# Kernel optimization log

Hardware: AMD Instinct MI355X
Metric: run time of the kernel (lower is better)

The kernel has to match this reference:

```python
import jax, jax.numpy as jnp
import numpy as np

B, N, D, H = 4, 1024, 768, 12
DH = D // H
HIDDEN = 4 * D
EPS = 1e-6


def _layernorm(x, g, b):
    mu = jnp.mean(x, axis=-1, keepdims=True)
    var = jnp.mean(jnp.square(x - mu), axis=-1, keepdims=True)
    return (x - mu) * jax.lax.rsqrt(var + EPS) * g + b


def setup_inputs() -> dict:
    key = jax.random.key(0)
    ks = jax.random.split(key, 8)
    s = 0.02  # init scale for weights
    return {
        "x": jax.random.normal(ks[0], (B, N, D), jnp.float32),
        "adj_bias": jax.random.normal(ks[1], (N, N), jnp.float32) * 0.1,
        "ln1_g": jnp.ones((D,), jnp.float32),
        "ln1_b": jnp.zeros((D,), jnp.float32),
        "qkv_w": jax.random.normal(ks[2], (D, 3 * D), jnp.float32) * s,
        "qkv_b": jnp.zeros((3 * D,), jnp.float32),
        "proj_w": jax.random.normal(ks[3], (D, D), jnp.float32) * s,
        "proj_b": jnp.zeros((D,), jnp.float32),
        "ln2_g": jnp.ones((D,), jnp.float32),
        "ln2_b": jnp.zeros((D,), jnp.float32),
        "fc1_w": jax.random.normal(ks[4], (D, HIDDEN), jnp.float32) * s,
        "fc1_b": jnp.zeros((HIDDEN,), jnp.float32),
        "fc2_w": jax.random.normal(ks[5], (HIDDEN, D), jnp.float32) * s,
        "fc2_b": jnp.zeros((D,), jnp.float32),
    }


def reference(x, adj_bias, ln1_g, ln1_b, qkv_w, qkv_b, proj_w, proj_b,
              ln2_g, ln2_b, fc1_w, fc1_b, fc2_w, fc2_b):
    scale = DH ** -0.5
    # --- attention with additive adjacency bias ---
    h = _layernorm(x, ln1_g, ln1_b)
    qkv = (h @ qkv_w + qkv_b).reshape(B, N, 3, H, DH)
    q, k, v = (jnp.moveaxis(qkv, 2, 0)[i].transpose(0, 2, 1, 3) for i in range(3))  # [B,H,N,DH]
    scores = jnp.einsum('bhqd,bhkd->bhqk', q, k) * scale + adj_bias[None, None]
    w = jax.nn.softmax(scores, axis=-1)
    attn = jnp.einsum('bhqk,bhkd->bhqd', w, v)          # [B,H,N,DH]
    attn = attn.transpose(0, 2, 1, 3).reshape(B, N, D)  # [B,N,D]
    x = x + (attn @ proj_w + proj_b)
    # --- MLP ---
    h2 = _layernorm(x, ln2_g, ln2_b)
    m = jax.nn.gelu(h2 @ fc1_w + fc1_b, approximate=False) @ fc2_w + fc2_b
    return x + m
```

## Files before the change

### kernel.cpp

```cpp
#include <hip/hip_runtime.h>
#include <cstdint>
#include <cstring>

typedef unsigned short u16;
typedef __attribute__((ext_vector_type(8))) short short8;
typedef __attribute__((ext_vector_type(4))) float float4v;

#define BB 4
#define NN 1024
#define DD 768
#define HH 12
#define DHH 64
#define HID 3072
#define MM (BB*NN)

__device__ __forceinline__ u16 f2b(float f) {
  unsigned int u = __float_as_uint(f);
  u += 0x7FFF + ((u >> 16) & 1);
  return (u16)(u >> 16);
}
__device__ __forceinline__ float b2f(u16 h) {
  return __uint_as_float(((unsigned int)h) << 16);
}

__device__ __forceinline__ void gll16(const void* g, void* l) {
  __builtin_amdgcn_global_load_lds(
      (const __attribute__((address_space(1))) unsigned int*)g,
      (__attribute__((address_space(3))) unsigned int*)l, 16, 0, 0);
}

__global__ __launch_bounds__(256)
void front_k(const float* __restrict__ qkvw, const float* __restrict__ projw,
             const float* __restrict__ fc1w, const float* __restrict__ fc2w,
             const float* __restrict__ adj, const float* __restrict__ x,
             const float* __restrict__ ln1g, const float* __restrict__ ln1b,
             u16* __restrict__ wtqkv, u16* __restrict__ wtproj,
             u16* __restrict__ wtfc1, u16* __restrict__ wtfc2,
             u16* __restrict__ adjP, u16* __restrict__ hbuf) {
  __shared__ float tile[32][33];
  __shared__ float rs[4], rs2[4], bc[2];
  const int id = blockIdx.x, t = threadIdx.x;
  if (id < 6912) {
    const float* w; u16* wt; int K, N, tid;
    if (id < 1728)      { w = qkvw;  wt = wtqkv;  K = DD;  N = 3 * DD; tid = id; }
    else if (id < 2304) { w = projw; wt = wtproj; K = DD;  N = DD;     tid = id - 1728; }
    else if (id < 4608) { w = fc1w;  wt = wtfc1;  K = DD;  N = HID;    tid = id - 2304; }
    else                { w = fc2w;  wt = wtfc2;  K = HID; N = DD;     tid = id - 4608; }
    const int ntiles = N / 32;
    const int n0 = (tid % ntiles) * 32, k0 = (tid / ntiles) * 32;
    const int tx = t & 31, ty = t >> 5;
#pragma unroll
    for (int i = 0; i < 4; i++)
      tile[ty + i * 8][tx] = w[(size_t)(k0 + ty + i * 8) * N + n0 + tx];
    __syncthreads();
#pragma unroll
    for (int i = 0; i < 4; i++)
      wt[(size_t)(n0 + ty + i * 8) * K + k0 + tx] = f2b(tile[tx][ty + i * 8]);
  } else if (id < 7168) {
    const int aid = id - 6912;
    const int qt = aid >> 4, kt = aid & 15;
    const int wv = t >> 6, q4 = (t >> 4) & 3, m15 = t & 15;
    u16 v[16];
#pragma unroll
    for (int ct = 0; ct < 4; ct++)
#pragma unroll
      for (int r = 0; r < 4; r++)
        v[ct * 4 + r] =
            f2b(adj[(size_t)(qt * 64 + wv * 16 + q4 * 4 + r) * NN + kt * 64 + ct * 16 + m15]);
    u16* dst = adjP + (size_t)aid * 4096 + t * 16;
    *(uint4*)dst = *(const uint4*)&v[0];
    *(uint4*)(dst + 8) = *(const uint4*)&v[8];
  } else {
    const int row = id - 7168;
    const float* xr = x + (size_t)row * DD;
    float v0 = xr[t], v1 = xr[t + 256], v2 = xr[t + 512];
    float s = v0 + v1 + v2;
    float s2 = v0 * v0 + v1 * v1 + v2 * v2;
#pragma unroll
    for (int off = 32; off > 0; off >>= 1) {
      s += __shfl_down(s, off);
      s2 += __shfl_down(s2, off);
    }
    const int lane = t & 63, wv = t >> 6;
    if (lane == 0) { rs[wv] = s; rs2[wv] = s2; }
    __syncthreads();
    if (t == 0) {
      float ts = rs[0] + rs[1] + rs[2] + rs[3];
      float ts2 = rs2[0] + rs2[1] + rs2[2] + rs2[3];
      float mean = ts * (1.f / DD);
      float var = ts2 * (1.f / DD) - mean * mean;
      bc[0] = mean;
      bc[1] = rsqrtf(var + 1e-6f);
    }
    __syncthreads();
    const float mean = bc[0], rstd = bc[1];
    u16* orow = hbuf + (size_t)row * DD;
    orow[t]       = f2b((v0 - mean) * rstd * ln1g[t]       + ln1b[t]);
    orow[t + 256] = f2b((v1 - mean) * rstd * ln1g[t + 256] + ln1b[t + 256]);
    orow[t + 512] = f2b((v2 - mean) * rstd * ln1g[t + 512] + ln1b[t + 512]);
  }
}

__global__ __launch_bounds__(256)
void ln_k(const float* __restrict__ x, const float* __restrict__ g,
          const float* __restrict__ b, u16* __restrict__ o) {
  const int row = blockIdx.x, t = threadIdx.x;
  const float* xr = x + (size_t)row * DD;
  float v0 = xr[t], v1 = xr[t + 256], v2 = xr[t + 512];
  float s = v0 + v1 + v2;
  float s2 = v0 * v0 + v1 * v1 + v2 * v2;
#pragma unroll
  for (int off = 32; off > 0; off >>= 1) {
    s += __shfl_down(s, off);
    s2 += __shfl_down(s2, off);
  }
  __shared__ float rs[4], rs2[4], bc[2];
  const int lane = t & 63, wv = t >> 6;
  if (lane == 0) { rs[wv] = s; rs2[wv] = s2; }
  __syncthreads();
  if (t == 0) {
    float ts = rs[0] + rs[1] + rs[2] + rs[3];
    float ts2 = rs2[0] + rs2[1] + rs2[2] + rs2[3];
    float mean = ts * (1.f / DD);
    float var = ts2 * (1.f / DD) - mean * mean;
    bc[0] = mean;
    bc[1] = rsqrtf(var + 1e-6f);
  }
  __syncthreads();
  const float mean = bc[0], rstd = bc[1];
  u16* orow = o + (size_t)row * DD;
  orow[t]       = f2b((v0 - mean) * rstd * g[t]       + b[t]);
  orow[t + 256] = f2b((v1 - mean) * rstd * g[t + 256] + b[t + 256]);
  orow[t + 512] = f2b((v2 - mean) * rstd * g[t + 512] + b[t + 512]);
}

template <int MODE, int TN, int BK, int NC>
__global__ __launch_bounds__(128, 2)
void gemm_k(const u16* __restrict__ A, const u16* __restrict__ Bt,
            const float* __restrict__ bias, const float* __restrict__ resid,
            float* __restrict__ outf, u16* __restrict__ outb,
            u16* __restrict__ outq, u16* __restrict__ outk, u16* __restrict__ outv,
            int K) {
  constexpr int BM = 64;
  __shared__ u16 As[2][BM * BK];
  __shared__ u16 Bs[2][TN * BK];
  constexpr int JM = TN / 32;
  constexpr int KK = BK / 32;
  constexpr int SLOTS = BK / 8;
  constexpr int AI = BM * SLOTS / 64;
  constexpr int BI = TN * SLOTS / 64;
  constexpr int VC = (AI + BI) / 2;
  constexpr int NB = NC / TN;
  constexpr int RN = NB / 2;
  constexpr int MB = MM / BM;

  const int id = blockIdx.x;
  const int xcd = id & 7, idx = id >> 3;
  const int tileN = ((xcd & 1) * RN + idx % RN) * TN;
  const int tileM = ((xcd >> 1) * (MB / 4) + idx / RN) * BM;

  const int lane = threadIdx.x & 63, wave = threadIdx.x >> 6;
  const int wcol = wave * (TN / 2);
  const int m15 = lane & 15, q4 = lane >> 4;
  const int rkey = (BK == 32) ? ((m15 >> 1) & 3) : (m15 & 7);

  float4v acc[4][JM];
#pragma unroll
  for (int i = 0; i < 4; i++)
#pragma unroll
    for (int j = 0; j < JM; j++) acc[i][j] = (float4v)0.f;

  auto stage = [&](int kt, int buf) {
    const int kk0 = kt * BK;
#pragma unroll
    for (int q = wave; q < AI; q += 2) {
      const int c = q * 64 + lane;
      const int row = c / SLOTS, slot = c % SLOTS;
      const int key = (BK == 32) ? ((row >> 1) & 3) : (row & 7);
      gll16(A + (size_t)(tileM + row) * K + kk0 + (slot ^ key) * 8, &As[buf][q * 512]);
    }
#pragma unroll
    for (int q = wave; q < BI; q += 2) {
      const int c = q * 64 + lane;
      const int row = c / SLOTS, slot = c % SLOTS;
      const int key = (BK == 32) ? ((row >> 1) & 3) : (row & 7);
      gll16(Bt + (size_t)(tileN + row) * K + kk0 + (slot ^ key) * 8, &Bs[buf][q * 512]);
    }
  };

  const int T = K / BK;
  stage(0, 0);
  for (int kt = 0; kt < T; ++kt) {
    const int cur = kt & 1;
    if (kt + 1 < T) {
      stage(kt + 1, cur ^ 1);
      asm volatile("s_waitcnt vmcnt(%0)\n\ts_barrier" :: "n"(VC) : "memory");
    } else {
      asm volatile("s_waitcnt vmcnt(0)\n\ts_barrier" ::: "memory");
    }
    short8 af[4][KK], bfr[JM][KK];
#pragma unroll
    for (int i = 0; i < 4; i++)
#pragma unroll
      for (int kk = 0; kk < KK; kk++)
        af[i][kk] = *(const short8*)(
            &As[cur][(i * 16 + m15) * BK + (((kk * 4 + q4) ^ rkey)) * 8]);
#pragma unroll
    for (int j = 0; j < JM; j++)
#pragma unroll
      for (int kk = 0; kk < KK; kk++)
        bfr[j][kk] = *(const short8*)(
            &Bs[cur][(wcol + j * 16 + m15) * BK + (((kk * 4 + q4) ^ rkey)) * 8]);
#pragma unroll
    for (int i = 0; i < 4; i++)
#pragma unroll
      for (int j = 0; j < JM; j++)
#pragma unroll
        for (int kk = 0; kk < KK; kk++)
          acc[i][j] =
              __builtin_amdgcn_mfma_f32_16x16x32_bf16(af[i][kk], bfr[j][kk], acc[i][j], 0, 0, 0);
    asm volatile("s_waitcnt lgkmcnt(0)\n\ts_barrier" ::: "memory");
  }

#pragma unroll
  for (int i = 0; i < 4; i++) {
#pragma unroll
    for (int j = 0; j < JM; j++) {
      const int col = tileN + wcol + j * 16 + m15;
#pragma unroll
      for (int r = 0; r < 4; r++) {
        const int row = tileM + i * 16 + q4 * 4 + r;
        float v = acc[i][j][r] + bias[col];
        if (MODE == 1) {
          outf[(size_t)row * NC + col] = resid[(size_t)row * NC + col] + v;
        } else if (MODE == 2) {
          float gv = 0.5f * v * (1.f + erff(v * 0.70710678f));
          outb[(size_t)row * NC + col] = f2b(gv);
        } else {
          const int three = col / DD, hh = (col % DD) >> 6, dh = col & 63;
          const int bb = row >> 10, nn = row & 1023;
          if (three == 2) {
            outv[(((size_t)(bb * HH + hh)) * DHH + dh) * NN + nn] = f2b(v);
          } else {
            const size_t idx2 = (((size_t)(bb * HH + hh)) * NN + nn) * DHH + dh;
            (three == 0 ? outq : outk)[idx2] = f2b(v);
          }
        }
      }
    }
  }
}

__global__ __launch_bounds__(256, 4)
void attn_k(const u16* __restrict__ qw, const u16* __restrict__ kw,
            const u16* __restrict__ vtw, const u16* __restrict__ adjP,
            u16* __restrict__ out) {
  __shared__ u16 Ks[64][72];
  __shared__ u16 Vt[64][72];
  __shared__ u16 Pb[4][16][72];

  const int id = blockIdx.x;
  const int bh = (id & 7) * 6 + ((id >> 3) >> 4);
  const int qt = (id >> 3) & 15;
  const int t = threadIdx.x, lane = t & 63, wave = t >> 6;
  const int m15 = lane & 15, q4 = lane >> 4;

  const u16* qrow = qw + ((size_t)bh * NN + qt * 64 + wave * 16 + m15) * DHH;
  const short8 qf0 = *(const short8*)(qrow + q4 * 8);
  const short8 qf1 = *(const short8*)(qrow + 32 + q4 * 8);

  float lreg[4] = {0.f, 0.f, 0.f, 0.f};
  float4v o[4];
#pragma unroll
  for (int ct = 0; ct < 4; ct++) o[ct] = (float4v)0.f;

  const u16* kbase0 = kw + (size_t)bh * NN * DHH;
  const u16* vtbase0 = vtw + (size_t)bh * DHH * NN;
  const u16* abase = adjP + (size_t)qt * 16 * 4096 + t * 16;

  const int r0 = t >> 3;
  const int c80 = (t & 7) * 8;

  uint4 kr0 = *(const uint4*)(kbase0 + r0 * 64 + c80);
  uint4 kr1 = *(const uint4*)(kbase0 + (r0 + 32) * 64 + c80);
  uint4 vr0 = *(const uint4*)(vtbase0 + (size_t)r0 * NN + c80);
  uint4 vr1 = *(const uint4*)(vtbase0 + (size_t)(r0 + 32) * NN + c80);

  for (int kt = 0; kt < 16; kt++) {
    __syncthreads();
    *(uint4*)&Ks[r0][c80] = kr0;
    *(uint4*)&Ks[r0 + 32][c80] = kr1;
    *(uint4*)&Vt[r0][c80] = vr0;
    *(uint4*)&Vt[r0 + 32][c80] = vr1;
    __syncthreads();
    if (kt < 15) {
      const u16* kb = kbase0 + (size_t)(kt + 1) * 64 * DHH;
      const u16* vb = vtbase0 + (kt + 1) * 64;
      kr0 = *(const uint4*)(kb + r0 * 64 + c80);
      kr1 = *(const uint4*)(kb + (r0 + 32) * 64 + c80);
      vr0 = *(const uint4*)(vb + (size_t)r0 * NN + c80);
      vr1 = *(const uint4*)(vb + (size_t)(r0 + 32) * NN + c80);
    }
    u16 av[16];
    const u16* ap = abase + (size_t)kt * 4096;
    *(uint4*)&av[0] = *(const uint4*)ap;
    *(uint4*)&av[8] = *(const uint4*)(ap + 8);

    float4v s[4];
#pragma unroll
    for (int ct = 0; ct < 4; ct++) s[ct] = (float4v)0.f;
#pragma unroll
    for (int ct = 0; ct < 4; ct++) {
      short8 b = *(const short8*)&Ks[ct * 16 + m15][q4 * 8];
      s[ct] = __builtin_amdgcn_mfma_f32_16x16x32_bf16(qf0, b, s[ct], 0, 0, 0);
    }
#pragma unroll
    for (int ct = 0; ct < 4; ct++) {
      short8 b = *(const short8*)&Ks[ct * 16 + m15][32 + q4 * 8];
      s[ct] = __builtin_amdgcn_mfma_f32_16x16x32_bf16(qf1, b, s[ct], 0, 0, 0);
    }

#pragma unroll
    for (int ct = 0; ct < 4; ct++)
#pragma unroll
      for (int r = 0; r < 4; r++) {
        float v = s[ct][r] * 0.125f + b2f(av[ct * 4 + r]);
        u16 pb = f2b(__expf(v));
        Pb[wave][q4 * 4 + r][ct * 16 + m15] = pb;
        lreg[r] += b2f(pb);
      }

    asm volatile("s_waitcnt lgkmcnt(0)" ::: "memory");

    short8 a0 = *(const short8*)&Pb[wave][m15][q4 * 8];
    short8 a1 = *(const short8*)&Pb[wave][m15][32 + q4 * 8];
#pragma unroll
    for (int ct = 0; ct < 4; ct++) {
      short8 b = *(const short8*)&Vt[ct * 16 + m15][q4 * 8];
      o[ct] = __builtin_amdgcn_mfma_f32_16x16x32_bf16(a0, b, o[ct], 0, 0, 0);
    }
#pragma unroll
    for (int ct = 0; ct < 4; ct++) {
      short8 b = *(const short8*)&Vt[ct * 16 + m15][32 + q4 * 8];
      o[ct] = __builtin_amdgcn_mfma_f32_16x16x32_bf16(a1, b, o[ct], 0, 0, 0);
    }
  }

#pragma unroll
  for (int off = 1; off < 16; off <<= 1)
#pragma unroll
    for (int r = 0; r < 4; r++) lreg[r] += __shfl_xor(lreg[r], off);

  const int bb2 = bh / HH, hh = bh % HH;
  const int row0 = qt * 64 + wave * 16 + q4 * 4;
#pragma unroll
  for (int ct = 0; ct < 4; ct++)
#pragma unroll
    for (int r = 0; r < 4; r++)
      out[((size_t)(bb2 * NN + row0 + r)) * DD + hh * 64 + ct * 16 + m15] =
          f2b(o[ct][r] / lreg[r]);
}

extern "C" void kernel_launch(void* const* d_in, const int* in_sizes, int n_in,
                              void* d_out, int out_size, void* d_ws, size_t ws_size,
                              hipStream_t stream) {
  const float* x     = (const float*)d_in[0];
  const float* adj   = (const float*)d_in[1];
  const float* ln1g  = (const float*)d_in[2];
  const float* ln1b  = (const float*)d_in[3];
  const float* qkvw  = (const float*)d_in[4];
  const float* qkvb  = (const float*)d_in[5];
  const float* projw = (const float*)d_in[6];
  const float* projb = (const float*)d_in[7];
  const float* ln2g  = (const float*)d_in[8];
  const float* ln2b  = (const float*)d_in[9];
  const float* fc1w  = (const float*)d_in[10];
  const float* fc1b  = (const float*)d_in[11];
  const float* fc2w  = (const float*)d_in[12];
  const float* fc2b  = (const float*)d_in[13];
  float* out = (float*)d_out;

  char* ws = (char*)d_ws;
  u16* wtqkv = (u16*)ws;  ws += (size_t)DD * (3 * DD) * 2;
  u16* wtproj = (u16*)ws; ws += (size_t)DD * DD * 2;
  u16* wtfc1 = (u16*)ws;  ws += (size_t)DD * HID * 2;
  u16* wtfc2 = (u16*)ws;  ws += (size_t)HID * DD * 2;
  u16* adjP = (u16*)ws;   ws += (size_t)NN * NN * 2;
  u16* hbuf = (u16*)ws;   ws += (size_t)MM * DD * 2;
  u16* qws = (u16*)ws;    ws += (size_t)MM * DD * 2;
  u16* kws = (u16*)ws;    ws += (size_t)MM * DD * 2;
  u16* vtws = (u16*)ws;   ws += (size_t)MM * DD * 2;
  u16* attnb = (u16*)ws;  ws += (size_t)MM * DD * 2;
  u16* h2buf = (u16*)ws;  ws += (size_t)MM * DD * 2;
  u16* a1buf = (u16*)ws;  ws += (size_t)MM * HID * 2;

  front_k<<<7168 + MM, 256, 0, stream>>>(qkvw, projw, fc1w, fc2w, adj, x, ln1g, ln1b,
                                         wtqkv, wtproj, wtfc1, wtfc2, adjP, hbuf);

  gemm_k<0, 128, 32, 3 * DD><<<((3 * DD) / 128) * (MM / 64), 128, 0, stream>>>(
      hbuf, wtqkv, qkvb, nullptr, nullptr, nullptr, qws, kws, vtws, DD);

  attn_k<<<(NN / 64) * (BB * HH), 256, 0, stream>>>(qws, kws, vtws, adjP, attnb);

  gemm_k<1, 64, 64, DD><<<(DD / 64) * (MM / 64), 128, 0, stream>>>(
      attnb, wtproj, projb, x, out, nullptr, nullptr, nullptr, nullptr, DD);

  ln_k<<<MM, 256, 0, stream>>>(out, ln2g, ln2b, h2buf);

  gemm_k<2, 128, 32, HID><<<(HID / 128) * (MM / 64), 128, 0, stream>>>(
      h2buf, wtfc1, fc1b, nullptr, nullptr, a1buf, nullptr, nullptr, nullptr, DD);

  gemm_k<1, 64, 64, DD><<<(DD / 64) * (MM / 64), 128, 0, stream>>>(
      a1buf, wtfc2, fc2b, out, out, nullptr, nullptr, nullptr, nullptr, HID);
}
```

Measured before the change: 274.1 us.

## Triple-buffer GEMM shared-memory tiles to prefetch two K-steps ahead

The GEMM main loop moves from double to triple buffering of the A and B shared-memory tiles. The loop is unrolled by three with rotating buffers, and the wait counts are set so that two tiles of global loads stay in flight while one tile is computed. The goal is to hide more global-load latency behind the MFMA work. In exchange it uses 1.5x the LDS per block, which may limit occupancy, and it assumes the number of K tiles is a multiple of three.

```diff
diff --git a/kernel.cpp b/kernel.cpp
--- a/kernel.cpp
+++ b/kernel.cpp
@@ -142,8 +142,8 @@
             u16* __restrict__ outq, u16* __restrict__ outk, u16* __restrict__ outv,
             int K) {
   constexpr int BM = 64;
-  __shared__ u16 As[2][BM * BK];
-  __shared__ u16 Bs[2][TN * BK];
+  __shared__ u16 As[3][BM * BK];
+  __shared__ u16 Bs[3][TN * BK];
   constexpr int JM = TN / 32;
   constexpr int KK = BK / 32;
   constexpr int SLOTS = BK / 8;
@@ -188,29 +188,20 @@
     }
   };
 
-  const int T = K / BK;
-  stage(0, 0);
-  for (int kt = 0; kt < T; ++kt) {
-    const int cur = kt & 1;
-    if (kt + 1 < T) {
-      stage(kt + 1, cur ^ 1);
-      asm volatile("s_waitcnt vmcnt(%0)\n\ts_barrier" :: "n"(VC) : "memory");
-    } else {
-      asm volatile("s_waitcnt vmcnt(0)\n\ts_barrier" ::: "memory");
-    }
+  auto compute = [&](int buf) {
     short8 af[4][KK], bfr[JM][KK];
 #pragma unroll
     for (int i = 0; i < 4; i++)
 #pragma unroll
       for (int kk = 0; kk < KK; kk++)
         af[i][kk] = *(const short8*)(
-            &As[cur][(i * 16 + m15) * BK + (((kk * 4 + q4) ^ rkey)) * 8]);
+            &As[buf][(i * 16 + m15) * BK + (((kk * 4 + q4) ^ rkey)) * 8]);
 #pragma unroll
     for (int j = 0; j < JM; j++)
 #pragma unroll
       for (int kk = 0; kk < KK; kk++)
         bfr[j][kk] = *(const short8*)(
-            &Bs[cur][(wcol + j * 16 + m15) * BK + (((kk * 4 + q4) ^ rkey)) * 8]);
+            &Bs[buf][(wcol + j * 16 + m15) * BK + (((kk * 4 + q4) ^ rkey)) * 8]);
 #pragma unroll
     for (int i = 0; i < 4; i++)
 #pragma unroll
@@ -219,8 +210,34 @@
         for (int kk = 0; kk < KK; kk++)
           acc[i][j] =
               __builtin_amdgcn_mfma_f32_16x16x32_bf16(af[i][kk], bfr[j][kk], acc[i][j], 0, 0, 0);
+  };
+
+  const int T = K / BK;
+  stage(0, 0);
+  stage(1, 1);
+  for (int kt = 0; kt < T - 3; kt += 3) {
+    stage(kt + 2, 2);
+    asm volatile("s_waitcnt vmcnt(%0)\n\ts_barrier" :: "n"(2 * VC) : "memory");
+    compute(0);
     asm volatile("s_waitcnt lgkmcnt(0)\n\ts_barrier" ::: "memory");
-  }
+    stage(kt + 3, 0);
+    asm volatile("s_waitcnt vmcnt(%0)\n\ts_barrier" :: "n"(2 * VC) : "memory");
+    compute(1);
+    asm volatile("s_waitcnt lgkmcnt(0)\n\ts_barrier" ::: "memory");
+    stage(kt + 4, 1);
+    asm volatile("s_waitcnt vmcnt(%0)\n\ts_barrier" :: "n"(2 * VC) : "memory");
+    compute(2);
+    asm volatile("s_waitcnt lgkmcnt(0)\n\ts_barrier" ::: "memory");
+  }
+  stage(T - 1, 2);
+  asm volatile("s_waitcnt vmcnt(%0)\n\ts_barrier" :: "n"(2 * VC) : "memory");
+  compute(0);
+  asm volatile("s_waitcnt lgkmcnt(0)\n\ts_barrier" ::: "memory");
+  asm volatile("s_waitcnt vmcnt(%0)\n\ts_barrier" :: "n"(VC) : "memory");
+  compute(1);
+  asm volatile("s_waitcnt lgkmcnt(0)\n\ts_barrier" ::: "memory");
+  asm volatile("s_waitcnt vmcnt(0)\n\ts_barrier" ::: "memory");
+  compute(2);
 
 #pragma unroll
   for (int i = 0; i < 4; i++) {
```

Result: slower. 284.1 us (+3.6%).

## Add 128x128-tile double-buffered MFMA GEMM for QKV and FC1 projections

Applied to the files above, without the earlier changes.

Introduces a new GEMM kernel with 128x128 output tiles, 4 waves each computing a 64x64 sub-tile, BK=64 double-buffered LDS staging with XOR swizzle, and XCD-aware block mapping. It replaces the previous 64-row tile GEMM for the QKV and FC1 matmuls. The goal is more data reuse per LDS load and fewer blocks, cutting global and LDS traffic per FLOP. The cost is more registers and LDS per block and lower occupancy, with fewer blocks to spread across CUs.

```diff
diff --git a/kernel.cpp b/kernel.cpp
--- a/kernel.cpp
+++ b/kernel.cpp
@@ -251,6 +251,109 @@
   }
 }
 
+template <int MODE, int NC>
+__global__ __launch_bounds__(256, 2)
+void gemm128_k(const u16* __restrict__ A, const u16* __restrict__ Bt,
+               const float* __restrict__ bias,
+               float* __restrict__ outf, u16* __restrict__ outb,
+               u16* __restrict__ outq, u16* __restrict__ outk, u16* __restrict__ outv,
+               int K) {
+  constexpr int BK = 64;
+  __shared__ u16 As[2][128 * BK];
+  __shared__ u16 Bs[2][128 * BK];
+  constexpr int NT = NC / 128;
+  constexpr int MT = MM / 128;
+  constexpr int RN = NT / 2;
+
+  const int id = blockIdx.x;
+  const int xcd = id & 7, idx = id >> 3;
+  const int tileN = ((xcd & 1) * RN + idx % RN) * 128;
+  const int tileM = ((xcd >> 1) * (MT / 4) + idx / RN) * 128;
+
+  const int t = threadIdx.x, lane = t & 63, wave = t >> 6;
+  const int mr = wave >> 1, nc = wave & 1;
+  const int m15 = lane & 15, q4 = lane >> 4;
+  const int rkey = m15 & 7;
+
+  float4v acc[4][4];
+#pragma unroll
+  for (int i = 0; i < 4; i++)
+#pragma unroll
+    for (int j = 0; j < 4; j++) acc[i][j] = (float4v)0.f;
+
+  auto stage = [&](int kt, int buf) {
+    const int kk0 = kt * BK;
+#pragma unroll
+    for (int q = wave; q < 16; q += 4) {
+      const int c = q * 64 + lane;
+      const int row = c >> 3, slot = c & 7;
+      gll16(A + (size_t)(tileM + row) * K + kk0 + (slot ^ (row & 7)) * 8, &As[buf][q * 512]);
+    }
+#pragma unroll
+    for (int q = wave; q < 16; q += 4) {
+      const int c = q * 64 + lane;
+      const int row = c >> 3, slot = c & 7;
+      gll16(Bt + (size_t)(tileN + row) * K + kk0 + (slot ^ (row & 7)) * 8, &Bs[buf][q * 512]);
+    }
+  };
+
+  const int T = K / BK;
+  stage(0, 0);
+  asm volatile("s_waitcnt vmcnt(0)\n\ts_barrier" ::: "memory");
+  for (int kt = 0; kt < T; ++kt) {
+    const int cur = kt & 1;
+    if (kt + 1 < T) stage(kt + 1, cur ^ 1);
+    short8 af[4][2], bfr[4][2];
+#pragma unroll
+    for (int i = 0; i < 4; i++)
+#pragma unroll
+      for (int kk = 0; kk < 2; kk++)
+        af[i][kk] = *(const short8*)(
+            &As[cur][(mr * 64 + i * 16 + m15) * BK + ((kk * 4 + q4) ^ rkey) * 8]);
+#pragma unroll
+    for (int j = 0; j < 4; j++)
+#pragma unroll
+      for (int kk = 0; kk < 2; kk++)
+        bfr[j][kk] = *(const short8*)(
+            &Bs[cur][(nc * 64 + j * 16 + m15) * BK + ((kk * 4 + q4) ^ rkey) * 8]);
+#pragma unroll
+    for (int i = 0; i < 4; i++)
+#pragma unroll
+      for (int j = 0; j < 4; j++)
+#pragma unroll
+        for (int kk = 0; kk < 2; kk++)
+          acc[i][j] =
+              __builtin_amdgcn_mfma_f32_16x16x32_bf16(af[i][kk], bfr[j][kk], acc[i][j], 0, 0, 0);
+    asm volatile("s_waitcnt vmcnt(0)\n\ts_barrier" ::: "memory");
+  }
+
+#pragma unroll
+  for (int i = 0; i < 4; i++) {
+#pragma unroll
+    for (int j = 0; j < 4; j++) {
+      const int col = tileN + nc * 64 + j * 16 + m15;
+#pragma unroll
+      for (int r = 0; r < 4; r++) {
+        const int row = tileM + mr * 64 + i * 16 + q4 * 4 + r;
+        float v = acc[i][j][r] + bias[col];
+        if (MODE == 2) {
+          float gv = 0.5f * v * (1.f + erff(v * 0.70710678f));
+          outb[(size_t)row * NC + col] = f2b(gv);
+        } else {
+          const int three = col / DD, hh = (col % DD) >> 6, dh = col & 63;
+          const int bb = row >> 10, nn = row & 1023;
+          if (three == 2) {
+            outv[(((size_t)(bb * HH + hh)) * DHH + dh) * NN + nn] = f2b(v);
+          } else {
+            const size_t idx2 = (((size_t)(bb * HH + hh)) * NN + nn) * DHH + dh;
+            (three == 0 ? outq : outk)[idx2] = f2b(v);
+          }
+        }
+      }
+    }
+  }
+}
+
 __global__ __launch_bounds__(256, 4)
 void attn_k(const u16* __restrict__ qw, const u16* __restrict__ kw,
             const u16* __restrict__ vtw, const u16* __restrict__ adjP,
@@ -397,8 +500,8 @@
   front_k<<<7168 + MM, 256, 0, stream>>>(qkvw, projw, fc1w, fc2w, adj, x, ln1g, ln1b,
                                          wtqkv, wtproj, wtfc1, wtfc2, adjP, hbuf);
 
-  gemm_k<0, 128, 32, 3 * DD><<<((3 * DD) / 128) * (MM / 64), 128, 0, stream>>>(
-      hbuf, wtqkv, qkvb, nullptr, nullptr, nullptr, qws, kws, vtws, DD);
+  gemm128_k<0, 3 * DD><<<((3 * DD) / 128) * (MM / 128), 256, 0, stream>>>(
+      hbuf, wtqkv, qkvb, nullptr, nullptr, qws, kws, vtws, DD);
 
   attn_k<<<(NN / 64) * (BB * HH), 256, 0, stream>>>(qws, kws, vtws, adjP, attnb);
 
@@ -407,8 +510,8 @@
 
   ln_k<<<MM, 256, 0, stream>>>(out, ln2g, ln2b, h2buf);
 
-  gemm_k<2, 128, 32, HID><<<(HID / 128) * (MM / 64), 128, 0, stream>>>(
-      h2buf, wtfc1, fc1b, nullptr, nullptr, a1buf, nullptr, nullptr, nullptr, DD);
+  gemm128_k<2, HID><<<(HID / 128) * (MM / 128), 256, 0, stream>>>(
+      h2buf, wtfc1, fc1b, nullptr, a1buf, nullptr, nullptr, nullptr, DD);
 
   gemm_k<1, 64, 64, DD><<<(DD / 64) * (MM / 64), 128, 0, stream>>>(
       a1buf, wtfc2, fc2b, out, out, nullptr, nullptr, nullptr, nullptr, HID);
```

Measured after the change: 278.2 us. Within noise of the previous version (+1.5%).
